# Kernel tuning notes

Measured on AMD Instinct MI355X. Metric: run time of the kernel, lower is better.

The kernel has to match this reference:

```python
import jax, jax.numpy as jnp
import numpy as np

N_NODES = 100000
N_EDGES = 3200000
IN_CH = 128
HID = 128
N_CLASSES = 32
N_GRAPHS = 256


def gcn_conv(x, W, b, src, dst, n_nodes):
    """PyG GCNConv: add self-loops, symmetric deg^-1/2 normalization,
    linear transform, gather-scatter aggregation, bias."""
    xw = x @ W  # [N, out]
    loop = jnp.arange(n_nodes, dtype=src.dtype)
    s = jnp.concatenate([src, loop])  # sources incl. self-loops
    d = jnp.concatenate([dst, loop])  # targets incl. self-loops
    deg = jax.ops.segment_sum(jnp.ones_like(d, dtype=xw.dtype), d,
                              num_segments=n_nodes)
    dinv = jnp.where(deg > 0, jax.lax.rsqrt(deg), 0.0)
    norm = dinv[s] * dinv[d]  # [E+N]
    msgs = xw[s] * norm[:, None]  # gather + scale
    out = jax.ops.segment_sum(msgs, d, num_segments=n_nodes)  # scatter-add
    return out + b


def global_mean_pool(x, batch, n_graphs):
    sums = jax.ops.segment_sum(x, batch, num_segments=n_graphs)
    cnt = jax.ops.segment_sum(jnp.ones((x.shape[0],), x.dtype), batch,
                              num_segments=n_graphs)
    return sums / jnp.maximum(cnt, 1.0)[:, None]


def setup_inputs() -> dict:
    key = jax.random.key(0)
    ks = jax.random.split(key, 9)
    x = jax.random.normal(ks[0], (N_NODES, IN_CH), dtype=jnp.float32)
    edge_index = jax.random.randint(ks[1], (2, N_EDGES), 0, N_NODES, dtype=jnp.int32)
    batch = jnp.sort(jax.random.randint(ks[2], (N_NODES,), 0, N_GRAPHS, dtype=jnp.int32))
    s1 = 1.0 / np.sqrt(IN_CH)
    s2 = 1.0 / np.sqrt(HID)
    W1 = jax.random.uniform(ks[3], (IN_CH, HID), jnp.float32, -s1, s1)
    b1 = jnp.zeros((HID,), jnp.float32)
    W2 = jax.random.uniform(ks[4], (HID, HID), jnp.float32, -s2, s2)
    b2 = jnp.zeros((HID,), jnp.float32)
    Wfc = jax.random.uniform(ks[5], (HID, N_CLASSES), jnp.float32, -s2, s2)
    bfc = jax.random.uniform(ks[6], (N_CLASSES,), jnp.float32, -s2, s2)
    return {"x": x, "edge_index": edge_index, "batch": batch,
            "W1": W1, "b1": b1, "W2": W2, "b2": b2, "Wfc": Wfc, "bfc": bfc}


def reference(x, edge_index, batch, W1, b1, W2, b2, Wfc, bfc):
    src, dst = edge_index[0], edge_index[1]
    h = jax.nn.relu(gcn_conv(x, W1, b1, src, dst, N_NODES))
    h = jax.nn.relu(gcn_conv(h, W2, b2, src, dst, N_NODES))
    g = global_mean_pool(h, batch, N_GRAPHS)  # [G, HID]
    return g @ Wfc + bfc  # [G, N_CLASSES]
```

## Files before the change

kernel.cpp:

```cpp
#include <hip/hip_runtime.h>
#include <hip/hip_bf16.h>
#include <hip/hip_fp16.h>

static constexpr int CH     = 128;
static constexpr int NCLS   = 32;
static constexpr int NGRAPH = 256;

static constexpr int BSHIFT = 8;
static constexpr int BW     = 1 << BSHIFT;
static constexpr int MAXB   = 512;

typedef _Float16 half8 __attribute__((ext_vector_type(8)));
typedef _Float16 half4 __attribute__((ext_vector_type(4)));
typedef float    f32x4 __attribute__((ext_vector_type(4)));
typedef float    f32x2 __attribute__((ext_vector_type(2)));

static constexpr float FP8_SCALE = 64.0f;
static constexpr float FP8_INV   = 1.0f / 64.0f;

__device__ __forceinline__ unsigned char enc8(float v) {
  return (unsigned char)(__builtin_amdgcn_cvt_pk_fp8_f32(v, v, 0, false) & 0xFF);
}

__global__ __launch_bounds__(1024) void k_scatter(
    const int* __restrict__ src, const int* __restrict__ dst,
    int* __restrict__ gcur, int* __restrict__ ebuf, int E, int CAP,
    int* __restrict__ xzero) {
  __shared__ int bcnt[MAXB];
  __shared__ int bbase[MAXB];
  int t = threadIdx.x;
  if (blockIdx.x == 0 && t < 32) xzero[t] = 0;
  if (t < MAXB) bcnt[t] = 0;
  __syncthreads();
  int base = blockIdx.x * 8192;
  int s_[8], d_[8], r_[8];
  #pragma unroll
  for (int j = 0; j < 8; ++j) {
    int i = base + j * 1024 + t;
    if (i < E) {
      s_[j] = src[i];
      d_[j] = dst[i];
      r_[j] = atomicAdd(&bcnt[d_[j] >> BSHIFT], 1);
    }
  }
  __syncthreads();
  if (t < MAXB && bcnt[t]) bbase[t] = atomicAdd(&gcur[t], bcnt[t]);
  __syncthreads();
  #pragma unroll
  for (int j = 0; j < 8; ++j) {
    int i = base + j * 1024 + t;
    if (i < E) {
      int b = d_[j] >> BSHIFT;
      int p = ((d_[j] & (BW - 1)) << 17) | s_[j];
      ebuf[b * CAP + bbase[b] + r_[j]] = p;
    }
  }
}

__global__ __launch_bounds__(1024) void k_build(
    const int* __restrict__ ebuf, const int* __restrict__ gcur,
    int* __restrict__ offs, int* __restrict__ oend,
    float* __restrict__ dinv, int* __restrict__ csr, int N, int CAP,
    const float* __restrict__ W1, const float* __restrict__ W2,
    _Float16* __restrict__ WhT1, _Float16* __restrict__ WhT2) {
  __shared__ int sdeg[BW];
  __shared__ int sscan[BW];
  int b = blockIdx.x;
  int t = threadIdx.x;

  int gi = b * 1024 + t;
  if (gi < 2 * CH * CH) {
    const float* W = (gi < CH * CH) ? W1 : W2;
    _Float16* T   = (gi < CH * CH) ? WhT1 : WhT2;
    int j = gi & (CH * CH - 1);
    int k = j >> 7, n = j & 127;
    T[n * CH + k] = (_Float16)W[j];
  }

  int lo = b << BSHIFT;
  int e0 = b * CAP;
  int e1 = e0 + gcur[b];

  if (t < BW) sdeg[t] = 0;
  __syncthreads();
  for (int e = e0 + t; e < e1; e += 1024)
    atomicAdd(&sdeg[ebuf[e] >> 17], 1);
  __syncthreads();
  if (t < BW) sscan[t] = (sdeg[t] + 3) & ~3;
  __syncthreads();
  for (int st = 1; st < BW; st <<= 1) {
    int v = (t < BW && t >= st) ? sscan[t - st] : 0;
    __syncthreads();
    if (t < BW) sscan[t] += v;
    __syncthreads();
  }
  if (t < BW) {
    int deg  = sdeg[t];
    int pdeg = (deg + 3) & ~3;
    int ex = b * CAP + sscan[t] - pdeg;
    int n = lo + t;
    if (n < N) {
      offs[n] = ex;
      oend[n] = ex + deg;
      dinv[n] = 1.0f / sqrtf((float)(deg + 1));
      for (int q = deg; q < pdeg; ++q) csr[ex + q] = N;
    }
    sscan[t] = ex;
  }
  __syncthreads();
  for (int e = e0 + t; e < e1; e += 1024) {
    int p = ebuf[e];
    int pos = atomicAdd(&sscan[p >> 17], 1);
    csr[pos] = p & 0x1FFFF;
  }
}

__device__ __forceinline__ void stage_w(const _Float16* __restrict__ WhT,
                                        _Float16 (*Ws)[136], int tid) {
  #pragma unroll
  for (int l = 0; l < 8; ++l) {
    int idx = tid + l * 256;
    int n = idx >> 4, k8 = (idx & 15) << 3;
    *(half8*)&Ws[n][k8] = *(const half8*)(WhT + n * CH + k8);
  }
}

__device__ __forceinline__ void gemm_core64(
    const _Float16 (*As)[136], const _Float16 (*Ws)[136],
    const float* __restrict__ dinv, unsigned char* __restrict__ C,
    int row0, int M, int tid) {
  int lane = tid & 63, wave = tid >> 6;
  int quad = lane >> 4, sub = lane & 15;
  int m0 = wave * 16;

  f32x4 acc[8];
  #pragma unroll
  for (int j = 0; j < 8; ++j) acc[j] = (f32x4){0.f, 0.f, 0.f, 0.f};

  #pragma unroll
  for (int kc = 0; kc < 4; ++kc) {
    int ko = kc * 32 + quad * 8;
    half8 a = *(const half8*)&As[m0 + sub][ko];
    #pragma unroll
    for (int nt = 0; nt < 8; ++nt) {
      half8 b = *(const half8*)&Ws[nt * 16 + sub][ko];
      acc[nt] = __builtin_amdgcn_mfma_f32_16x16x32_f16(a, b, acc[nt], 0, 0, 0);
    }
  }
  #pragma unroll
  for (int r = 0; r < 4; ++r) {
    int row = row0 + m0 + quad * 4 + r;
    if (row < M) {
      float d = dinv[row] * FP8_SCALE;
      #pragma unroll
      for (int nt = 0; nt < 8; ++nt)
        C[(size_t)row * CH + nt * 16 + sub] = enc8(acc[nt][r] * d);
    }
  }
}

__global__ __launch_bounds__(256) void k_gemm_f32(
    const float* __restrict__ A, const _Float16* __restrict__ WhT,
    const float* __restrict__ dinv, unsigned char* __restrict__ C, int M) {
  __shared__ _Float16 As[64][136];
  __shared__ _Float16 Ws[128][136];
  int tid = threadIdx.x;
  int row0 = blockIdx.x * 64;
  #pragma unroll
  for (int l = 0; l < 8; ++l) {
    int idx = tid + l * 256;
    int r = idx >> 5, c4 = (idx & 31) << 2;
    int rr = row0 + r; if (rr >= M) rr = M - 1;
    float4 v = *(const float4*)(A + (size_t)rr * CH + c4);
    half4 hv = { (_Float16)v.x, (_Float16)v.y, (_Float16)v.z, (_Float16)v.w };
    *(half4*)&As[r][c4] = hv;
  }
  stage_w(WhT, Ws, tid);
  __syncthreads();
  gemm_core64(As, Ws, dinv, C, row0, M, tid);
}

__global__ __launch_bounds__(256) void k_gemm_f16(
    const _Float16* __restrict__ A, const _Float16* __restrict__ WhT,
    const float* __restrict__ dinv, unsigned char* __restrict__ C, int M) {
  __shared__ _Float16 As[64][136];
  __shared__ _Float16 Ws[128][136];
  int tid = threadIdx.x;
  int row0 = blockIdx.x * 64;
  #pragma unroll
  for (int l = 0; l < 4; ++l) {
    int idx = tid + l * 256;
    int r = idx >> 4, c8 = (idx & 15) << 3;
    int rr = row0 + r; if (rr >= M) rr = M - 1;
    *(half8*)&As[r][c8] = *(const half8*)(A + (size_t)rr * CH + c8);
  }
  stage_w(WhT, Ws, tid);
  __syncthreads();
  gemm_core64(As, Ws, dinv, C, row0, M, tid);
}

__global__ __launch_bounds__(256) void k_agg(
    const unsigned int* __restrict__ xs32, const int* __restrict__ csr,
    const int* __restrict__ offs, const int* __restrict__ oend,
    const float* __restrict__ dinv, const float* __restrict__ bias,
    __half* __restrict__ out, int N) {
  int lane  = threadIdx.x & 63;
  int wid0  = blockIdx.x * 4 + (threadIdx.x >> 6);
  int wstep = gridDim.x * 4;
  int e = lane >> 5;
  unsigned int c = lane & 31;
  float4 bb = *(const float4*)(bias + c * 4);

  auto G = [&](int s) -> unsigned int {
    return xs32[((unsigned int)s << 5) | c];
  };

  for (int wid = wid0; wid * 2 < N; wid += wstep) {
    int nA = wid * 2, nB = nA + 1;
    bool hasB = (nB < N);

    int eA = offs[nA];
    int cA = (oend[nA] - eA + 3) >> 2;
    int eB = hasB ? offs[nB] : eA;
    int cB = hasB ? ((oend[nB] - eB + 3) >> 2) : 0;

    f32x2 a0 = {0.f, 0.f}, a1 = {0.f, 0.f};
    f32x2 b0 = {0.f, 0.f}, b1 = {0.f, 0.f};
    if (e == 0) {
      unsigned int ow = G(nA);
      a0 = __builtin_amdgcn_cvt_pk_f32_fp8((int)ow, false);
      a1 = __builtin_amdgcn_cvt_pk_f32_fp8((int)ow, true);
      if (hasB) {
        unsigned int ob = G(nB);
        b0 = __builtin_amdgcn_cvt_pk_f32_fp8((int)ob, false);
        b1 = __builtin_amdgcn_cvt_pk_f32_fp8((int)ob, true);
      }
    }

    #define ACC(d, x0, x1) \
      x0 += __builtin_amdgcn_cvt_pk_f32_fp8((int)(d), false); \
      x1 += __builtin_amdgcn_cvt_pk_f32_fp8((int)(d), true);

    if (cA >= 2 && cB >= 2) {
      int4 ca0 = *(const int4*)(csr + eA);
      int4 ca1 = *(const int4*)(csr + eA + 4);
      int4 cb0 = *(const int4*)(csr + eB);
      int4 cb1 = *(const int4*)(csr + eB + 4);
      do {
        int sA0 = e ? ca0.y : ca0.x, sA1 = e ? ca0.w : ca0.z;
        int sA2 = e ? ca1.y : ca1.x, sA3 = e ? ca1.w : ca1.z;
        int sB0 = e ? cb0.y : cb0.x, sB1 = e ? cb0.w : cb0.z;
        int sB2 = e ? cb1.y : cb1.x, sB3 = e ? cb1.w : cb1.z;
        unsigned int dA0 = G(sA0), dA1 = G(sA1), dA2 = G(sA2), dA3 = G(sA3);
        unsigned int dB0 = G(sB0), dB1 = G(sB1), dB2 = G(sB2), dB3 = G(sB3);
        eA += 8; eB += 8; cA -= 2; cB -= 2;
        int4 na0 = *(const int4*)(csr + eA);
        int4 na1 = *(const int4*)(csr + eA + 4);
        int4 nb0 = *(const int4*)(csr + eB);
        int4 nb1 = *(const int4*)(csr + eB + 4);
        ACC(dA0, a0, a1); ACC(dA1, a0, a1); ACC(dA2, a0, a1); ACC(dA3, a0, a1);
        ACC(dB0, b0, b1); ACC(dB1, b0, b1); ACC(dB2, b0, b1); ACC(dB3, b0, b1);
        ca0 = na0; ca1 = na1; cb0 = nb0; cb1 = nb1;
      } while (cA >= 2 && cB >= 2);
    }

    auto drain = [&](int ee, int cc, f32x2& x0, f32x2& x1) {
      while (cc >= 2) {
        int4 q0 = *(const int4*)(csr + ee);
        int4 q1 = *(const int4*)(csr + ee + 4);
        int s0 = e ? q0.y : q0.x, s1 = e ? q0.w : q0.z;
        int s2 = e ? q1.y : q1.x, s3 = e ? q1.w : q1.z;
        unsigned int d0 = G(s0), d1 = G(s1), d2 = G(s2), d3 = G(s3);
        ACC(d0, x0, x1); ACC(d1, x0, x1); ACC(d2, x0, x1); ACC(d3, x0, x1);
        ee += 8; cc -= 2;
      }
      if (cc > 0) {
        int4 q0 = *(const int4*)(csr + ee);
        int s0 = e ? q0.y : q0.x, s1 = e ? q0.w : q0.z;
        unsigned int d0 = G(s0), d1 = G(s1);
        ACC(d0, x0, x1); ACC(d1, x0, x1);
      }
    };
    drain(eA, cA, a0, a1);
    if (hasB) drain(eB, cB, b0, b1);
    #undef ACC

    a0[0] += __shfl_xor(a0[0], 32); a0[1] += __shfl_xor(a0[1], 32);
    a1[0] += __shfl_xor(a1[0], 32); a1[1] += __shfl_xor(a1[1], 32);
    if (hasB) {
      b0[0] += __shfl_xor(b0[0], 32); b0[1] += __shfl_xor(b0[1], 32);
      b1[0] += __shfl_xor(b1[0], 32); b1[1] += __shfl_xor(b1[1], 32);
    }

    if (e == 0) {
      {
        float dn = dinv[nA] * FP8_INV;
        float r0 = fmaf(a0[0], dn, bb.x), r1 = fmaf(a0[1], dn, bb.y);
        float r2 = fmaf(a1[0], dn, bb.z), r3 = fmaf(a1[1], dn, bb.w);
        __half2 h0 = __floats2half2_rn(fmaxf(r0, 0.f), fmaxf(r1, 0.f));
        __half2 h1 = __floats2half2_rn(fmaxf(r2, 0.f), fmaxf(r3, 0.f));
        __half2* op = (__half2*)(out + (size_t)nA * CH + c * 4);
        op[0] = h0; op[1] = h1;
      }
      if (hasB) {
        float dn = dinv[nB] * FP8_INV;
        float r0 = fmaf(b0[0], dn, bb.x), r1 = fmaf(b0[1], dn, bb.y);
        float r2 = fmaf(b1[0], dn, bb.z), r3 = fmaf(b1[1], dn, bb.w);
        __half2 h0 = __floats2half2_rn(fmaxf(r0, 0.f), fmaxf(r1, 0.f));
        __half2 h1 = __floats2half2_rn(fmaxf(r2, 0.f), fmaxf(r3, 0.f));
        __half2* op = (__half2*)(out + (size_t)nB * CH + c * 4);
        op[0] = h0; op[1] = h1;
      }
    }
  }
}

__global__ __launch_bounds__(256) void k_poolfc(
    const __half* __restrict__ h, const int* __restrict__ batch,
    const float* __restrict__ Wfc, const float* __restrict__ bfc,
    float* __restrict__ outp, int N) {
  __shared__ float sred[256][2];
  __shared__ float gs[CH];
  int g = blockIdx.x;
  int t = threadIdx.x;

  int lo = 0, hi = N;
  while (lo < hi) { int m = (lo + hi) >> 1; if (batch[m] < g) lo = m + 1; else hi = m; }
  int s0 = lo;
  hi = N;
  while (lo < hi) { int m = (lo + hi) >> 1; if (batch[m] < g + 1) lo = m + 1; else hi = m; }
  int s1 = lo;

  int ch2 = t & 63;
  int rh  = t >> 6;
  const __half2* h2 = (const __half2*)h;
  float ax = 0.f, ay = 0.f;
  for (int n = s0 + rh; n < s1; n += 4) {
    float2 v = __half22float2(h2[(size_t)n * 64 + ch2]);
    ax += v.x; ay += v.y;
  }
  sred[t][0] = ax; sred[t][1] = ay;
  __syncthreads();
  if (t < 64) {
    float invc = 1.0f / fmaxf((float)(s1 - s0), 1.0f);
    float sx = sred[t][0] + sred[t + 64][0] + sred[t + 128][0] + sred[t + 192][0];
    float sy = sred[t][1] + sred[t + 64][1] + sred[t + 128][1] + sred[t + 192][1];
    gs[2 * t]     = sx * invc;
    gs[2 * t + 1] = sy * invc;
  }
  __syncthreads();
  if (t < NCLS) {
    float acc = bfc[t];
    #pragma unroll 8
    for (int cc = 0; cc < CH; ++cc)
      acc = fmaf(gs[cc], Wfc[cc * NCLS + t], acc);
    outp[g * NCLS + t] = acc;
  }
}

extern "C" void kernel_launch(void* const* d_in, const int* in_sizes, int n_in,
                              void* d_out, int out_size, void* d_ws, size_t ws_size,
                              hipStream_t stream) {
  const float* x    = (const float*)d_in[0];
  const int*   ei   = (const int*)d_in[1];
  const int*   batch= (const int*)d_in[2];
  const float* W1   = (const float*)d_in[3];
  const float* b1   = (const float*)d_in[4];
  const float* W2   = (const float*)d_in[5];
  const float* b2   = (const float*)d_in[6];
  const float* Wfc  = (const float*)d_in[7];
  const float* bfc  = (const float*)d_in[8];
  float* outp = (float*)d_out;

  const int N = in_sizes[0] / CH;
  const int E = in_sizes[1] / 2;
  const int* src = ei;
  const int* dst = ei + E;
  const int NBUCK = (N + BW - 1) >> BSHIFT;
  int CAP = (E / NBUCK) + (E / NBUCK) / 8 + 1280;
  CAP = (CAP + 3) & ~3;

  char* w = (char*)d_ws;
  size_t o = 0;
  auto carve = [&](size_t bytes) -> void* {
    o = (o + 255) & ~(size_t)255;
    void* p = w + o;
    o += bytes;
    return p;
  };
  int*      offs   = (int*)     carve((size_t)N * 4);
  int*      oendb  = (int*)     carve((size_t)N * 4);
  int*      gcur   = (int*)     carve(MAXB * 4);
  int*      csr    = (int*)     carve((size_t)NBUCK * CAP * 4);
  float*    dinv   = (float*)   carve((size_t)N * 4);
  _Float16* WhT1   = (_Float16*)carve((size_t)CH * CH * 2);
  _Float16* WhT2   = (_Float16*)carve((size_t)CH * CH * 2);
  unsigned char* xsbuf = (unsigned char*)carve((size_t)(N + 1) * CH);
  __half*   hbuf   = (__half*)  carve((size_t)N * CH * 2);
  (void)ws_size;

  int* ebuf = (int*)hbuf;

  (void)hipMemsetAsync(gcur, 0, MAXB * 4, stream);

  const int GB64 = (N + 63) / 64;
  int AB = (N + 7) / 8;
  if (AB > 2048) AB = 2048;

  k_scatter<<<(E + 8191) / 8192, 1024, 0, stream>>>(
      src, dst, gcur, ebuf, E, CAP, (int*)(xsbuf + (size_t)N * CH));
  k_build<<<NBUCK, 1024, 0, stream>>>(ebuf, gcur, offs, oendb, dinv, csr,
                                      N, CAP, W1, W2, WhT1, WhT2);

  k_gemm_f32<<<GB64, 256, 0, stream>>>(x, WhT1, dinv, xsbuf, N);
  k_agg<<<AB, 256, 0, stream>>>((const unsigned int*)xsbuf, csr, offs, oendb,
                                dinv, b1, hbuf, N);
  k_gemm_f16<<<GB64, 256, 0, stream>>>((const _Float16*)hbuf, WhT2, dinv, xsbuf, N);
  k_agg<<<AB, 256, 0, stream>>>((const unsigned int*)xsbuf, csr, offs, oendb,
                                dinv, b2, hbuf, N);

  k_poolfc<<<NGRAPH, 256, 0, stream>>>(hbuf, batch, Wfc, bfc, outp, N);
  (void)out_size; (void)n_in;
}
```

Baseline: 333.4 us.

## Locally sort edges in shared memory before scatter; persistent GEMM with register A fragments

The edge scatter and CSR build kernels now counting-sort each chunk in shared memory by bucket/node before writing to global memory, so global writes become contiguous runs instead of random scattered stores. The GEMM kernels drop the shared A tile and instead load A fragments directly into registers in a grid-stride persistent loop over 16-row tiles, with a fixed 1024-block grid so the W staging is amortized across many tiles. This adds extra shared-memory scans and barriers and larger LDS usage, which may lower occupancy in the build kernels.

```diff
diff --git a/kernel.cpp b/kernel.cpp
--- a/kernel.cpp
+++ b/kernel.cpp
@@ -27,33 +27,51 @@
     int* __restrict__ gcur, int* __restrict__ ebuf, int E, int CAP,
     int* __restrict__ xzero) {
   __shared__ int bcnt[MAXB];
+  __shared__ int lofs[MAXB];
   __shared__ int bbase[MAXB];
+  __shared__ int sorted[8192];
+  __shared__ unsigned short sbkt[8192];
   int t = threadIdx.x;
   if (blockIdx.x == 0 && t < 32) xzero[t] = 0;
   if (t < MAXB) bcnt[t] = 0;
   __syncthreads();
   int base = blockIdx.x * 8192;
-  int s_[8], d_[8], r_[8];
+  int cnt = E - base; if (cnt > 8192) cnt = 8192;
+  int p_[8], b_[8], r_[8];
   #pragma unroll
   for (int j = 0; j < 8; ++j) {
-    int i = base + j * 1024 + t;
-    if (i < E) {
-      s_[j] = src[i];
-      d_[j] = dst[i];
-      r_[j] = atomicAdd(&bcnt[d_[j] >> BSHIFT], 1);
-    }
-  }
-  __syncthreads();
+    int i = j * 1024 + t;
+    if (i < cnt) {
+      int s = src[base + i], d = dst[base + i];
+      b_[j] = d >> BSHIFT;
+      p_[j] = ((d & (BW - 1)) << 17) | s;
+      r_[j] = atomicAdd(&bcnt[b_[j]], 1);
+    }
+  }
+  __syncthreads();
+  if (t < MAXB) lofs[t] = bcnt[t];
+  __syncthreads();
+  for (int st = 1; st < MAXB; st <<= 1) {
+    int v = (t < MAXB && t >= st) ? lofs[t - st] : 0;
+    __syncthreads();
+    if (t < MAXB) lofs[t] += v;
+    __syncthreads();
+  }
   if (t < MAXB && bcnt[t]) bbase[t] = atomicAdd(&gcur[t], bcnt[t]);
   __syncthreads();
   #pragma unroll
   for (int j = 0; j < 8; ++j) {
-    int i = base + j * 1024 + t;
-    if (i < E) {
-      int b = d_[j] >> BSHIFT;
-      int p = ((d_[j] & (BW - 1)) << 17) | s_[j];
-      ebuf[b * CAP + bbase[b] + r_[j]] = p;
-    }
+    int i = j * 1024 + t;
+    if (i < cnt) {
+      int pos = lofs[b_[j]] - bcnt[b_[j]] + r_[j];
+      sorted[pos] = p_[j];
+      sbkt[pos] = (unsigned short)b_[j];
+    }
+  }
+  __syncthreads();
+  for (int i = t; i < cnt; i += 1024) {
+    int bk = sbkt[i];
+    ebuf[bk * CAP + bbase[bk] + (i - (lofs[bk] - bcnt[bk]))] = sorted[i];
   }
 }
 
@@ -65,6 +83,11 @@
     _Float16* __restrict__ WhT1, _Float16* __restrict__ WhT2) {
   __shared__ int sdeg[BW];
   __shared__ int sscan[BW];
+  __shared__ int cur[BW];
+  __shared__ int chist[BW];
+  __shared__ int clofs[BW];
+  __shared__ int lsorted[8192];
+  __shared__ unsigned char lnode[8192];
   int b = blockIdx.x;
   int t = threadIdx.x;
 
@@ -79,12 +102,12 @@
 
   int lo = b << BSHIFT;
   int e0 = b * CAP;
-  int e1 = e0 + gcur[b];
+  int CNT = gcur[b];
 
   if (t < BW) sdeg[t] = 0;
   __syncthreads();
-  for (int e = e0 + t; e < e1; e += 1024)
-    atomicAdd(&sdeg[ebuf[e] >> 17], 1);
+  for (int i = t; i < CNT; i += 1024)
+    atomicAdd(&sdeg[ebuf[e0 + i] >> 17], 1);
   __syncthreads();
   if (t < BW) sscan[t] = (sdeg[t] + 3) & ~3;
   __syncthreads();
@@ -104,14 +127,52 @@
       oend[n] = ex + deg;
       dinv[n] = 1.0f / sqrtf((float)(deg + 1));
       for (int q = deg; q < pdeg; ++q) csr[ex + q] = N;
-    }
-    sscan[t] = ex;
-  }
-  __syncthreads();
-  for (int e = e0 + t; e < e1; e += 1024) {
-    int p = ebuf[e];
-    int pos = atomicAdd(&sscan[p >> 17], 1);
-    csr[pos] = p & 0x1FFFF;
+      cur[t] = ex;
+    }
+  }
+  __syncthreads();
+
+  for (int c0 = 0; c0 < CNT; c0 += 8192) {
+    int ccnt = CNT - c0; if (ccnt > 8192) ccnt = 8192;
+    if (t < BW) chist[t] = 0;
+    __syncthreads();
+    int p_[8], nd_[8], r_[8];
+    #pragma unroll
+    for (int j = 0; j < 8; ++j) {
+      int i = j * 1024 + t;
+      if (i < ccnt) {
+        p_[j] = ebuf[e0 + c0 + i];
+        nd_[j] = p_[j] >> 17;
+        r_[j] = atomicAdd(&chist[nd_[j]], 1);
+      }
+    }
+    __syncthreads();
+    if (t < BW) clofs[t] = chist[t];
+    __syncthreads();
+    for (int st = 1; st < BW; st <<= 1) {
+      int v = (t < BW && t >= st) ? clofs[t - st] : 0;
+      __syncthreads();
+      if (t < BW) clofs[t] += v;
+      __syncthreads();
+    }
+    #pragma unroll
+    for (int j = 0; j < 8; ++j) {
+      int i = j * 1024 + t;
+      if (i < ccnt) {
+        int pos = clofs[nd_[j]] - chist[nd_[j]] + r_[j];
+        lsorted[pos] = p_[j];
+        lnode[pos] = (unsigned char)nd_[j];
+      }
+    }
+    __syncthreads();
+    for (int i = t; i < ccnt; i += 1024) {
+      int nd = lnode[i];
+      int gpos = cur[nd] + (i - (clofs[nd] - chist[nd]));
+      csr[gpos] = lsorted[i] & 0x1FFFF;
+    }
+    __syncthreads();
+    if (t < BW) cur[t] += chist[t];
+    __syncthreads();
   }
 }
 
@@ -125,36 +186,29 @@
   }
 }
 
-__device__ __forceinline__ void gemm_core64(
-    const _Float16 (*As)[136], const _Float16 (*Ws)[136],
+__device__ __forceinline__ void gemm_tile(
+    const _Float16 (*Ws)[136], const half8* af,
     const float* __restrict__ dinv, unsigned char* __restrict__ C,
-    int row0, int M, int tid) {
-  int lane = tid & 63, wave = tid >> 6;
-  int quad = lane >> 4, sub = lane & 15;
-  int m0 = wave * 16;
-
+    int tile, int M, int quad, int sub) {
   f32x4 acc[8];
   #pragma unroll
   for (int j = 0; j < 8; ++j) acc[j] = (f32x4){0.f, 0.f, 0.f, 0.f};
-
   #pragma unroll
   for (int kc = 0; kc < 4; ++kc) {
-    int ko = kc * 32 + quad * 8;
-    half8 a = *(const half8*)&As[m0 + sub][ko];
     #pragma unroll
     for (int nt = 0; nt < 8; ++nt) {
-      half8 b = *(const half8*)&Ws[nt * 16 + sub][ko];
-      acc[nt] = __builtin_amdgcn_mfma_f32_16x16x32_f16(a, b, acc[nt], 0, 0, 0);
+      half8 b = *(const half8*)&Ws[nt * 16 + sub][kc * 32 + quad * 8];
+      acc[nt] = __builtin_amdgcn_mfma_f32_16x16x32_f16(af[kc], b, acc[nt], 0, 0, 0);
     }
   }
   #pragma unroll
   for (int r = 0; r < 4; ++r) {
-    int row = row0 + m0 + quad * 4 + r;
-    if (row < M) {
-      float d = dinv[row] * FP8_SCALE;
+    int orow = tile * 16 + quad * 4 + r;
+    if (orow < M) {
+      float d = dinv[orow] * FP8_SCALE;
       #pragma unroll
       for (int nt = 0; nt < 8; ++nt)
-        C[(size_t)row * CH + nt * 16 + sub] = enc8(acc[nt][r] * d);
+        C[(size_t)orow * CH + nt * 16 + sub] = enc8(acc[nt][r] * d);
     }
   }
 }
@@ -162,41 +216,51 @@
 __global__ __launch_bounds__(256) void k_gemm_f32(
     const float* __restrict__ A, const _Float16* __restrict__ WhT,
     const float* __restrict__ dinv, unsigned char* __restrict__ C, int M) {
-  __shared__ _Float16 As[64][136];
   __shared__ _Float16 Ws[128][136];
   int tid = threadIdx.x;
-  int row0 = blockIdx.x * 64;
-  #pragma unroll
-  for (int l = 0; l < 8; ++l) {
-    int idx = tid + l * 256;
-    int r = idx >> 5, c4 = (idx & 31) << 2;
-    int rr = row0 + r; if (rr >= M) rr = M - 1;
-    float4 v = *(const float4*)(A + (size_t)rr * CH + c4);
-    half4 hv = { (_Float16)v.x, (_Float16)v.y, (_Float16)v.z, (_Float16)v.w };
-    *(half4*)&As[r][c4] = hv;
-  }
   stage_w(WhT, Ws, tid);
   __syncthreads();
-  gemm_core64(As, Ws, dinv, C, row0, M, tid);
+  int lane = tid & 63;
+  int quad = lane >> 4, sub = lane & 15;
+  int ntiles = (M + 15) >> 4;
+  int wid0 = blockIdx.x * 4 + (tid >> 6);
+  int wstep = gridDim.x * 4;
+  for (int tile = wid0; tile < ntiles; tile += wstep) {
+    int row = tile * 16 + sub; if (row >= M) row = M - 1;
+    const float* arow = A + (size_t)row * CH + quad * 8;
+    half8 af[4];
+    #pragma unroll
+    for (int kc = 0; kc < 4; ++kc) {
+      float4 v0 = *(const float4*)(arow + kc * 32);
+      float4 v1 = *(const float4*)(arow + kc * 32 + 4);
+      af[kc] = (half8){(_Float16)v0.x, (_Float16)v0.y, (_Float16)v0.z, (_Float16)v0.w,
+                       (_Float16)v1.x, (_Float16)v1.y, (_Float16)v1.z, (_Float16)v1.w};
+    }
+    gemm_tile(Ws, af, dinv, C, tile, M, quad, sub);
+  }
 }
 
 __global__ __launch_bounds__(256) void k_gemm_f16(
     const _Float16* __restrict__ A, const _Float16* __restrict__ WhT,
     const float* __restrict__ dinv, unsigned char* __restrict__ C, int M) {
-  __shared__ _Float16 As[64][136];
   __shared__ _Float16 Ws[128][136];
   int tid = threadIdx.x;
-  int row0 = blockIdx.x * 64;
-  #pragma unroll
-  for (int l = 0; l < 4; ++l) {
-    int idx = tid + l * 256;
-    int r = idx >> 4, c8 = (idx & 15) << 3;
-    int rr = row0 + r; if (rr >= M) rr = M - 1;
-    *(half8*)&As[r][c8] = *(const half8*)(A + (size_t)rr * CH + c8);
-  }
   stage_w(WhT, Ws, tid);
   __syncthreads();
-  gemm_core64(As, Ws, dinv, C, row0, M, tid);
+  int lane = tid & 63;
+  int quad = lane >> 4, sub = lane & 15;
+  int ntiles = (M + 15) >> 4;
+  int wid0 = blockIdx.x * 4 + (tid >> 6);
+  int wstep = gridDim.x * 4;
+  for (int tile = wid0; tile < ntiles; tile += wstep) {
+    int row = tile * 16 + sub; if (row >= M) row = M - 1;
+    const _Float16* arow = A + (size_t)row * CH + quad * 8;
+    half8 af[4];
+    #pragma unroll
+    for (int kc = 0; kc < 4; ++kc)
+      af[kc] = *(const half8*)(arow + kc * 32);
+    gemm_tile(Ws, af, dinv, C, tile, M, quad, sub);
+  }
 }
 
 __global__ __launch_bounds__(256) void k_agg(
@@ -403,7 +467,7 @@
 
   (void)hipMemsetAsync(gcur, 0, MAXB * 4, stream);
 
-  const int GB64 = (N + 63) / 64;
+  const int GBW = 1024;
   int AB = (N + 7) / 8;
   if (AB > 2048) AB = 2048;
 
@@ -412,10 +476,10 @@
   k_build<<<NBUCK, 1024, 0, stream>>>(ebuf, gcur, offs, oendb, dinv, csr,
                                       N, CAP, W1, W2, WhT1, WhT2);
 
-  k_gemm_f32<<<GB64, 256, 0, stream>>>(x, WhT1, dinv, xsbuf, N);
+  k_gemm_f32<<<GBW, 256, 0, stream>>>(x, WhT1, dinv, xsbuf, N);
   k_agg<<<AB, 256, 0, stream>>>((const unsigned int*)xsbuf, csr, offs, oendb,
                                 dinv, b1, hbuf, N);
-  k_gemm_f16<<<GB64, 256, 0, stream>>>((const _Float16*)hbuf, WhT2, dinv, xsbuf, N);
+  k_gemm_f16<<<GBW, 256, 0, stream>>>((const _Float16*)hbuf, WhT2, dinv, xsbuf, N);
   k_agg<<<AB, 256, 0, stream>>>((const unsigned int*)xsbuf, csr, offs, oendb,
                                 dinv, b2, hbuf, N);
 
```

Result: no change. 326.9 us (-2.0%).
